# Kernel optimization log

Hardware: AMD Instinct MI355X
Metric: run time of the kernel (lower is better)

Reference implementation:

```python
import jax, jax.numpy as jnp
import numpy as np

IMG = 224          # image_size
FMAP = (56, 56)    # feature_map_dims (AdaptiveAvgPool2d((56,56)))
K_REWEIGHT = 3     # self.n_reweight
BLUR_RADIUS = 4    # KNNGaussianBlur(4): kernel 9, sigma 4


def _cdist(a, b):
    # Euclidean pairwise distance, [Na, D] x [Nb, D] -> [Na, Nb]
    a2 = jnp.sum(a * a, axis=1, keepdims=True)            # [Na,1]
    b2 = jnp.sum(b * b, axis=1, keepdims=True).T          # [1,Nb]
    d2 = a2 + b2 - 2.0 * (a @ b.T)
    return jnp.sqrt(jnp.maximum(d2, 0.0))


def _gaussian_blur(x):
    # x: [1,1,H,W]; torchvision GaussianBlur(kernel=9, sigma=4), reflect pad
    r, sigma = BLUR_RADIUS, float(BLUR_RADIUS)
    t = jnp.arange(2 * r + 1, dtype=x.dtype) - r
    g = jnp.exp(-(t * t) / (2.0 * sigma * sigma))
    g = g / jnp.sum(g)
    k2d = jnp.outer(g, g)[None, None]                     # [1,1,9,9]
    xp = jnp.pad(x, ((0, 0), (0, 0), (r, r), (r, r)), mode='reflect')
    return jax.lax.conv_general_dilated(
        xp, k2d, window_strides=(1, 1), padding='VALID',
        dimension_numbers=('NCHW', 'OIHW', 'NCHW'))


def setup_inputs() -> dict:
    key = jax.random.key(0)
    k1, k2 = jax.random.split(key)
    patch = jax.random.normal(k1, (FMAP[0] * FMAP[1], 768), dtype=jnp.float32)
    patch_lib = jax.random.normal(k2, (16384, 768), dtype=jnp.float32)
    mean = jnp.zeros((), dtype=jnp.float32)
    std = jnp.ones((), dtype=jnp.float32)
    return {"patch": patch, "patch_lib": patch_lib, "mean": mean, "std": std}


def reference(patch, patch_lib, mean, std):
    # normalization (method_name != 'Point_MAE' branch)
    p = (patch - mean) / std                               # [N, D]

    dist = _cdist(p, patch_lib)                            # [N, Nlib]
    min_val = jnp.min(dist, axis=1)                        # [N]
    min_idx = jnp.argmin(dist, axis=1)                     # [N]
    s_idx = jnp.argmax(min_val)
    s_star = jnp.max(min_val)

    m_test = p[s_idx]                                      # [D]
    m_star = patch_lib[min_idx[s_idx]]                     # [D]

    # distances of m_star to whole bank, k smallest
    w_dist = jnp.sqrt(jnp.maximum(
        jnp.sum((patch_lib - m_star) ** 2, axis=1), 0.0))  # [Nlib]
    _, nn_idx = jax.lax.top_k(-w_dist, K_REWEIGHT)         # smallest k
    m_star_knn = jnp.linalg.norm(
        m_test[None, :] - patch_lib[nn_idx[1:]], axis=1)   # [k-1]

    D_sqrt = jnp.sqrt(jnp.asarray(patch.shape[1], dtype=p.dtype))
    w = 1.0 - jnp.exp(s_star / D_sqrt) / jnp.sum(jnp.exp(m_star_knn / D_sqrt))
    s = w * s_star

    s_map = min_val.reshape(1, 1, *FMAP)
    s_map = jax.image.resize(s_map, (1, 1, IMG, IMG), method='bilinear')
    s_map = _gaussian_blur(s_map)
    return s, s_map
```

## Files before the change

### kernel.cpp

```cpp
#include <hip/hip_runtime.h>
#include <hip/hip_bf16.h>
#include <stdint.h>

#define N_PATCH 3136
#define N_PATCH_PAD 3328
#define N_LIB   16384
#define DIM     768
#define IMGSZ   224
#define FM      56

#define TILE 256
#define KT2 12
#define MT 13
#define NTILES 64

#define TAILB 64
#define D2_MARGIN 8.0f

typedef __bf16 bf16_t;
typedef __bf16 bf16x8 __attribute__((ext_vector_type(8)));
typedef __bf16 bf16x4_v __attribute__((ext_vector_type(4)));
typedef float  f32x4  __attribute__((ext_vector_type(4)));

#define FLT_MAX_ 3.402823466e+38f

struct Scal {
  unsigned long long approx_max_pack;
  unsigned long long cand_pack[64];
  int cand[64];
  int cand_count;
  int bar[4];
  int work;
};

__device__ __forceinline__ float wave_reduce_sum(float v) {
#pragma unroll
  for (int s = 32; s > 0; s >>= 1) v += __shfl_xor(v, s, 64);
  return v;
}

__device__ __forceinline__ float wave_reduce_min(float v) {
#pragma unroll
  for (int s = 32; s > 0; s >>= 1) v = fminf(v, __shfl_xor(v, s, 64));
  return v;
}

__device__ __forceinline__ unsigned long long shfl_xor_u64(unsigned long long v, int mask) {
  unsigned lo = (unsigned)v, hi = (unsigned)(v >> 32);
  lo = __shfl_xor(lo, mask, 64);
  hi = __shfl_xor(hi, mask, 64);
  return ((unsigned long long)hi << 32) | lo;
}

__device__ __forceinline__ void async16(const bf16_t* g, bf16_t* l) {
  __builtin_amdgcn_global_load_lds(
      (const __attribute__((address_space(1))) unsigned int*)g,
      (__attribute__((address_space(3))) unsigned int*)l, 16, 0, 0);
}

__device__ __forceinline__ void grid_bar(int* ctr, int nb) {
  __syncthreads();
  if (threadIdx.x == 0) {
    __threadfence();
    atomicAdd(ctr, 1);
    while (atomicAdd(ctr, 0) < nb) __builtin_amdgcn_s_sleep(8);
    __threadfence();
  }
  __syncthreads();
}

__device__ __forceinline__ float bf16u_to_f(unsigned short u) {
  return __uint_as_float(((unsigned)u) << 16);
}

__global__ void prep_kernel(const float* __restrict__ patch, const float* __restrict__ lib,
                            const float* __restrict__ meanp, const float* __restrict__ stdp,
                            bf16_t* __restrict__ pb, bf16_t* __restrict__ lb,
                            float* __restrict__ a2, float* __restrict__ b2, Scal* sc) {
  int t = threadIdx.x;
  int lane = t & 63;
  if (blockIdx.x == 0) {
    if (t < 64) sc->cand_pack[t] = ~0ULL;
    if (t == 64) { sc->approx_max_pack = 0ULL; sc->cand_count = 0; }
    if (t >= 65 && t < 69) sc->bar[t - 65] = 0;
    if (t == 69) sc->work = 0;
  }
  if (blockIdx.x < N_PATCH_PAD / 4) {
    int row = blockIdx.x * 4 + (t >> 6);
    if (row < N_PATCH) {
      float mu = meanp[0], sd = stdp[0];
      float acc = 0.f;
#pragma unroll
      for (int k = 0; k < 3; k++) {
        float4 v = ((const float4*)(patch + (size_t)row * DIM))[lane + 64 * k];
        v.x = (v.x - mu) / sd; v.y = (v.y - mu) / sd;
        v.z = (v.z - mu) / sd; v.w = (v.w - mu) / sd;
        bf16x4_v o = {(__bf16)v.x, (__bf16)v.y, (__bf16)v.z, (__bf16)v.w};
        *(bf16x4_v*)(pb + (size_t)row * DIM + (lane + 64 * k) * 4) = o;
        acc += v.x*v.x + v.y*v.y + v.z*v.z + v.w*v.w;
      }
      acc = wave_reduce_sum(acc);
      if (lane == 0) a2[row] = acc;
    } else {
      bf16x4_v z = {(__bf16)0.f, (__bf16)0.f, (__bf16)0.f, (__bf16)0.f};
#pragma unroll
      for (int k = 0; k < 3; k++)
        *(bf16x4_v*)(pb + (size_t)row * DIM + (lane + 64 * k) * 4) = z;
    }
  } else {
    int row = (blockIdx.x - N_PATCH_PAD / 4) * 4 + (t >> 6);
    float acc = 0.f;
#pragma unroll
    for (int k = 0; k < 3; k++) {
      float4 v = ((const float4*)(lib + (size_t)row * DIM))[lane + 64 * k];
      bf16x4_v o = {(__bf16)v.x, (__bf16)v.y, (__bf16)v.z, (__bf16)v.w};
      *(bf16x4_v*)(lb + (size_t)row * DIM + (lane + 64 * k) * 4) = o;
      acc += v.x*v.x + v.y*v.y + v.z*v.z + v.w*v.w;
    }
    acc = wave_reduce_sum(acc);
    if (lane == 0) b2[row] = acc;
  }
}

__global__ __launch_bounds__(512, 2)
void gemm_min_kernel(const bf16_t* __restrict__ pb, const bf16_t* __restrict__ lb,
                     const float* __restrict__ a2, const float* __restrict__ b2,
                     float* __restrict__ part) {
  __shared__ __align__(16) bf16_t As[2][2][128 * 64];
  __shared__ __align__(16) bf16_t Bs[2][2][128 * 64];

  const int t = threadIdx.x;
  const int wave = t >> 6;
  const int lane = t & 63;
  const int l15 = lane & 15;
  const int quad = lane >> 4;
  const int wm = (wave >> 2) * 128;
  const int wn = (wave & 3) * 64;
  const int mhw = wm >> 7;
  const int nhw = wn >> 7;
  const int wni = wn & 64;

  const int L0 = t >> 3;
  const int k0 = (t & 7) ^ (L0 & 7);
  const int sl0 = (((0 * 4 + quad) ^ (l15 & 7)) << 4);
  const int sl1 = (((1 * 4 + quad) ^ (l15 & 7)) << 4);

  const int x = blockIdx.x & 7;
  const int sblk = blockIdx.x >> 3;
  const int nt = x * 8 + (sblk & 7);
  const int n0 = nt * TILE;

  for (int g = 0; g < 4; ++g) {
    if (g * 32 + sblk >= 104) break;
    const int mt = g * 4 + (sblk >> 3);
    const int m0 = mt * TILE;

    __syncthreads();

    const bf16_t* gA = pb + (size_t)(m0 + L0) * DIM + k0 * 8;
    const bf16_t* gB = lb + (size_t)(n0 + L0) * DIM + k0 * 8;

    auto stageT = [&](int tk) {
      bf16_t* dA0 = &As[tk & 1][0][0];
      bf16_t* dA1 = &As[tk & 1][1][0];
      bf16_t* dB0 = &Bs[tk & 1][0][0];
      bf16_t* dB1 = &Bs[tk & 1][1][0];
      const bf16_t* sA = gA + tk * 64;
      const bf16_t* sB = gB + tk * 64;
      async16(sA,                       dA0 + t * 8);
      async16(sA + (size_t)64  * DIM,   dA0 + 4096 + t * 8);
      async16(sA + (size_t)128 * DIM,   dA1 + t * 8);
      async16(sA + (size_t)192 * DIM,   dA1 + 4096 + t * 8);
      async16(sB,                       dB0 + t * 8);
      async16(sB + (size_t)64  * DIM,   dB0 + 4096 + t * 8);
      async16(sB + (size_t)128 * DIM,   dB1 + t * 8);
      async16(sB + (size_t)192 * DIM,   dB1 + 4096 + t * 8);
    };

    f32x4 acc[8][4];
#pragma unroll
    for (int mi = 0; mi < 8; mi++)
#pragma unroll
      for (int ni = 0; ni < 4; ni++) { f32x4 z = {0.f,0.f,0.f,0.f}; acc[mi][ni] = z; }

    auto computeTile = [&](int d) {
      const char* Ab = (const char*)&As[d][mhw][0];
      const char* Bb = (const char*)&Bs[d][nhw][0];
      bf16x8 bfr[4][2];
#pragma unroll
      for (int ni = 0; ni < 4; ni++) {
        int lr = wni + ni * 16 + l15;
        bfr[ni][0] = *(const bf16x8*)(Bb + lr * 128 + sl0);
        bfr[ni][1] = *(const bf16x8*)(Bb + lr * 128 + sl1);
      }
#pragma unroll
      for (int q = 0; q < 4; q++) {
        bf16x8 aq[2][2];
#pragma unroll
        for (int mi = 0; mi < 2; mi++) {
          int lr = q * 32 + mi * 16 + l15;
          aq[mi][0] = *(const bf16x8*)(Ab + lr * 128 + sl0);
          aq[mi][1] = *(const bf16x8*)(Ab + lr * 128 + sl1);
        }
        __builtin_amdgcn_s_setprio(1);
#pragma unroll
        for (int mi = 0; mi < 2; mi++)
#pragma unroll
          for (int ni = 0; ni < 4; ni++) {
            acc[q*2+mi][ni] = __builtin_amdgcn_mfma_f32_16x16x32_bf16(
                aq[mi][0], bfr[ni][0], acc[q*2+mi][ni], 0, 0, 0);
            acc[q*2+mi][ni] = __builtin_amdgcn_mfma_f32_16x16x32_bf16(
                aq[mi][1], bfr[ni][1], acc[q*2+mi][ni], 0, 0, 0);
          }
        __builtin_amdgcn_s_setprio(0);
      }
    };

    stageT(0);
    for (int tk = 0; tk < KT2; ++tk) {
      asm volatile("s_waitcnt vmcnt(0) lgkmcnt(0)" ::: "memory");
      __builtin_amdgcn_s_barrier();
      asm volatile("" ::: "memory");
      if (tk + 1 < KT2) stageT(tk + 1);
      computeTile(tk & 1);
    }

    __syncthreads();
    unsigned* smin = (unsigned*)&As[0][0][0];
    if (t < 256) smin[t] = 0xffffffffu;
    __syncthreads();

    float b2n[4];
#pragma unroll
    for (int ni = 0; ni < 4; ni++) b2n[ni] = b2[n0 + wn + ni * 16 + l15];

#pragma unroll
    for (int mi = 0; mi < 8; mi++) {
#pragma unroll
      for (int r = 0; r < 4; r++) {
        int rloc = wm + mi * 16 + quad * 4 + r;
        int mrow = m0 + rloc;
        float a2v = a2[mrow < N_PATCH ? mrow : (N_PATCH - 1)];
        float best = a2v + b2n[0] - 2.0f * acc[mi][0][r];
#pragma unroll
        for (int ni = 1; ni < 4; ni++)
          best = fminf(best, a2v + b2n[ni] - 2.0f * acc[mi][ni][r]);
        best = fmaxf(best, 0.0f);
#pragma unroll
        for (int s = 1; s < 16; s <<= 1)
          best = fminf(best, __shfl_xor(best, s, 64));
        if (l15 == 0) atomicMin(&smin[rloc], __float_as_uint(best));
      }
    }
    __syncthreads();
    if (t < 256) part[(size_t)(m0 + t) * NTILES + nt] = __uint_as_float(smin[t]);
  }
}

__device__ __forceinline__ void wave_pick(const Scal* sc, int cnt, int lane,
                                          int* srow, float* sstar, int* ms) {
  unsigned long long pk = 0ULL;
  int rowv = 0, msv = 0;
  if (lane < cnt) {
    unsigned long long cp = sc->cand_pack[lane];
    rowv = sc->cand[lane];
    msv = (int)(cp & 0xffffffffu);
    pk = (cp & 0xffffffff00000000ULL) | (unsigned)(0xffffffffu - (unsigned)rowv);
  }
  unsigned long long m = pk;
#pragma unroll
  for (int s = 1; s < 64; s <<= 1) {
    unsigned long long o = shfl_xor_u64(m, s);
    if (o > m) m = o;
  }
  unsigned long long mask = __ballot(pk == m && lane < cnt);
  int wl = (int)(__ffsll((long long)mask) - 1);
  *srow = __shfl(rowv, wl, 64);
  *ms   = __shfl(msv, wl, 64);
  *sstar = sqrtf(__uint_as_float((unsigned)(m >> 32)));
}

__global__ __launch_bounds__(256, 2)
void tail_kernel(const float* __restrict__ part, float* __restrict__ min_val,
                 const float* __restrict__ patch, const float* __restrict__ lib,
                 const bf16_t* __restrict__ lb,
                 const float* __restrict__ meanp, const float* __restrict__ stdp,
                 Scal* __restrict__ sc, float* __restrict__ wdist2,
                 float* __restrict__ out0, float* __restrict__ outmap) {
  __shared__ union {
    unsigned long long sl[768];
    float rs[40 * 40];
  } sm;
  __shared__ float redbuf[4];
  __shared__ unsigned long long rb64[4];
  __shared__ int s_cnt;

  const int t = threadIdx.x;
  const int b = blockIdx.x;
  const int wave = t >> 6, lane = t & 63;

  {
    unsigned long long mp = 0ULL;
    for (int i = wave; i < 256; i += 4) {
      int row = b * 256 + i;
      if (row >= N_PATCH) break;
      float v = part[(size_t)row * NTILES + lane];
      v = wave_reduce_min(v);
      if (lane == 0) {
        float sv = sqrtf(v);
        min_val[row] = sv;
        unsigned long long cand = (((unsigned long long)__float_as_uint(sv)) << 32) |
                                  (unsigned)(0xffffffffu - (unsigned)row);
        if (cand > mp) mp = cand;
      }
    }
    if (lane == 0) rb64[wave] = mp;
    __syncthreads();
    if (t == 0) {
      unsigned long long mm = rb64[0];
      if (rb64[1] > mm) mm = rb64[1];
      if (rb64[2] > mm) mm = rb64[2];
      if (rb64[3] > mm) mm = rb64[3];
      if (mm) atomicMax(&sc->approx_max_pack, mm);
    }
  }
  grid_bar(&sc->bar[0], TAILB);

  if (b == 0) {
    float amax = __uint_as_float((unsigned)(atomicMax(&sc->approx_max_pack, 0ULL) >> 32));
    for (int i = t; i < N_PATCH; i += 256) {
      if (min_val[i] >= amax - 0.05f) {
        int p = atomicAdd(&sc->cand_count, 1);
        if (p < 64) sc->cand[p] = i;
      }
    }
  }
  grid_bar(&sc->bar[1], TAILB);

  if (t == 0) s_cnt = atomicAdd(&sc->cand_count, 0);
  __syncthreads();
  int cnt = s_cnt; if (cnt > 64) cnt = 64;

  {
    float mu = meanp[0], sd = stdp[0];
    for (int c = 0; c < cnt; c++) {
      int row = sc->cand[c];
      float pv_ = (t < NTILES) ? part[(size_t)row * NTILES + t] : FLT_MAX_;
      pv_ = wave_reduce_min(pv_);
      if (lane == 0) redbuf[wave] = pv_;
      __syncthreads();
      float bmin = fminf(fminf(redbuf[0], redbuf[1]), fminf(redbuf[2], redbuf[3]));
      __syncthreads();

      float4 pv[3];
#pragma unroll
      for (int k = 0; k < 3; k++) {
        float4 v = ((const float4*)(patch + (size_t)row * DIM))[lane + 64 * k];
        v.x = (v.x - mu) / sd; v.y = (v.y - mu) / sd;
        v.z = (v.z - mu) / sd; v.w = (v.w - mu) / sd;
        pv[k] = v;
      }
      int nt = b;
      float pmin = part[(size_t)row * NTILES + nt];
      if (pmin <= bmin + D2_MARGIN) {
        unsigned long long best = ~0ULL;
        int jb = nt * 256 + wave * 64;
        for (int rr = 0; rr < 64; rr++) {
          int j = jb + rr;
          const float4* pl = (const float4*)(lib + (size_t)j * DIM);
          float acc = 0.f;
#pragma unroll
          for (int k = 0; k < 3; k++) {
            float4 l = pl[lane + 64 * k];
            float dx = pv[k].x - l.x, dy = pv[k].y - l.y;
            float dz = pv[k].z - l.z, dw = pv[k].w - l.w;
            acc += dx*dx + dy*dy + dz*dz + dw*dw;
          }
          acc = wave_reduce_sum(acc);
          unsigned long long pk = (((unsigned long long)__float_as_uint(acc)) << 32) | (unsigned)j;
          if (pk < best) best = pk;
        }
        if (lane == 0) atomicMin(&sc->cand_pack[c], best);
      }
    }
  }
  grid_bar(&sc->bar[2], TAILB);

  {
    int srow_, ms; float ss_;
    wave_pick(sc, cnt, lane, &srow_, &ss_, &ms);
    float pm[12];
    const ushort4* pms = (const ushort4*)(lb + (size_t)ms * DIM);
#pragma unroll
    for (int k = 0; k < 3; k++) {
      ushort4 u = pms[lane + 64 * k];
      pm[k*4+0] = bf16u_to_f(u.x); pm[k*4+1] = bf16u_to_f(u.y);
      pm[k*4+2] = bf16u_to_f(u.z); pm[k*4+3] = bf16u_to_f(u.w);
    }
    int jbase = b * 256 + wave * 64;
    for (int rr = 0; rr < 64; rr += 2) {
      int j0 = jbase + rr, j1 = j0 + 1;
      const ushort4* r0 = (const ushort4*)(lb + (size_t)j0 * DIM);
      const ushort4* r1 = (const ushort4*)(lb + (size_t)j1 * DIM);
      float a0 = 0.f, a1 = 0.f;
#pragma unroll
      for (int k = 0; k < 3; k++) {
        ushort4 u0 = r0[lane + 64 * k];
        ushort4 u1 = r1[lane + 64 * k];
        float d;
        d = bf16u_to_f(u0.x) - pm[k*4+0]; a0 += d * d;
        d = bf16u_to_f(u0.y) - pm[k*4+1]; a0 += d * d;
        d = bf16u_to_f(u0.z) - pm[k*4+2]; a0 += d * d;
        d = bf16u_to_f(u0.w) - pm[k*4+3]; a0 += d * d;
        d = bf16u_to_f(u1.x) - pm[k*4+0]; a1 += d * d;
        d = bf16u_to_f(u1.y) - pm[k*4+1]; a1 += d * d;
        d = bf16u_to_f(u1.z) - pm[k*4+2]; a1 += d * d;
        d = bf16u_to_f(u1.w) - pm[k*4+3]; a1 += d * d;
      }
      a0 = wave_reduce_sum(a0);
      a1 = wave_reduce_sum(a1);
      if (lane == 0) { wdist2[j0] = a0; wdist2[j1] = a1; }
    }
  }
  grid_bar(&sc->bar[3], TAILB);

  if (b == 0) {
    unsigned long long b0 = ~0ULL, b1 = ~0ULL, b2 = ~0ULL;
    for (int j = t; j < N_LIB; j += 256) {
      unsigned long long pk = (((unsigned long long)__float_as_uint(wdist2[j])) << 32) | (unsigned)j;
      if (pk < b0)      { b2 = b1; b1 = b0; b0 = pk; }
      else if (pk < b1) { b2 = b1; b1 = pk; }
      else if (pk < b2) { b2 = pk; }
    }
    sm.sl[t * 3 + 0] = b0; sm.sl[t * 3 + 1] = b1; sm.sl[t * 3 + 2] = b2;
    __syncthreads();
    if (t >= 64) return;

    unsigned long long c0 = ~0ULL, c1 = ~0ULL, c2 = ~0ULL;
#pragma unroll
    for (int e = 0; e < 12; e++) {
      unsigned long long pk = sm.sl[t * 12 + e];
      if (pk < c0)      { c2 = c1; c1 = c0; c0 = pk; }
      else if (pk < c1) { c2 = c1; c1 = pk; }
      else if (pk < c2) { c2 = pk; }
    }
    unsigned long long res1 = 0, res2 = 0;
#pragma unroll
    for (int r = 0; r < 3; r++) {
      unsigned long long m = c0;
#pragma unroll
      for (int s = 1; s < 64; s <<= 1) {
        unsigned long long o = shfl_xor_u64(m, s);
        if (o < m) m = o;
      }
      if (r == 1) res1 = m;
      if (r == 2) res2 = m;
      if (c0 == m) { c0 = c1; c1 = c2; c2 = ~0ULL; }
    }
    int nA = (int)(res1 & 0xffffffffu);
    int nB = (int)(res2 & 0xffffffffu);

    int srow, ms2; float sstar;
    wave_pick(sc, cnt, t, &srow, &sstar, &ms2);

    float mu = meanp[0], sd = stdp[0];
    float accA = 0.f, accB = 0.f;
#pragma unroll
    for (int k = 0; k < 3; k++) {
      float4 p4 = ((const float4*)(patch + (size_t)srow * DIM))[t + 64 * k];
      float4 a4 = ((const float4*)(lib + (size_t)nA * DIM))[t + 64 * k];
      float4 b4 = ((const float4*)(lib + (size_t)nB * DIM))[t + 64 * k];
      float px = (p4.x - mu) / sd, py = (p4.y - mu) / sd;
      float pz = (p4.z - mu) / sd, pw = (p4.w - mu) / sd;
      float dax = px - a4.x, day = py - a4.y, daz = pz - a4.z, daw = pw - a4.w;
      float dbx = px - b4.x, dby = py - b4.y, dbz = pz - b4.z, dbw = pw - b4.w;
      accA += dax*dax + day*day + daz*daz + daw*daw;
      accB += dbx*dbx + dby*dby + dbz*dbz + dbw*dbw;
    }
    accA = wave_reduce_sum(accA);
    accB = wave_reduce_sum(accB);
    if (t == 0) {
      float dsq = sqrtf((float)DIM);
      float d1 = sqrtf(accA), d2v = sqrtf(accB);
      float w = 1.0f - expf(sstar / dsq) / (expf(d1 / dsq) + expf(d2v / dsq));
      out0[0] = w * sstar;
    }
    return;
  }

  if (b > 49) return;
  {
    int tile = b - 1;
    int bx = tile % 7, by = tile / 7;
    int ox0 = bx * 32, oy0 = by * 32;

    for (int i = t; i < 1600; i += 256) {
      int ly = i / 40, lx = i % 40;
      int gy = oy0 - 4 + ly; gy = gy < 0 ? 0 : (gy > 223 ? 223 : gy);
      int gx = ox0 - 4 + lx; gx = gx < 0 ? 0 : (gx > 223 ? 223 : gx);
      float sy = fminf(fmaxf(0.25f * gy - 0.375f, 0.0f), 55.0f);
      float sx = fminf(fmaxf(0.25f * gx - 0.375f, 0.0f), 55.0f);
      int y0 = (int)sy; if (y0 > 54) y0 = 54;
      int x0 = (int)sx; if (x0 > 54) x0 = 54;
      float fy = sy - y0, fx = sx - x0;
      float v00 = min_val[y0*FM + x0],     v01 = min_val[y0*FM + x0 + 1];
      float v10 = min_val[(y0+1)*FM + x0], v11 = min_val[(y0+1)*FM + x0 + 1];
      float a = v00 + fx * (v01 - v00);
      float bb = v10 + fx * (v11 - v10);
      sm.rs[i] = a + fy * (bb - a);
    }
    __syncthreads();

    float g[9]; float gs = 0.f;
#pragma unroll
    for (int i = 0; i < 9; i++) { float tt = (float)(i - 4); g[i] = expf(-(tt*tt)/32.0f); gs += g[i]; }
#pragma unroll
    for (int i = 0; i < 9; i++) g[i] /= gs;

    for (int p = t; p < 1024; p += 256) {
      int y = oy0 + p / 32, x = ox0 + (p & 31);
      float acc = 0.f;
#pragma unroll
      for (int dy = 0; dy < 9; dy++) {
        int yy = y + dy - 4;
        yy = yy < 0 ? -yy : (yy > IMGSZ - 1 ? 2*(IMGSZ-1) - yy : yy);
        int lyy = yy - (oy0 - 4);
        float ra = 0.f;
#pragma unroll
        for (int dx = 0; dx < 9; dx++) {
          int xx = x + dx - 4;
          xx = xx < 0 ? -xx : (xx > IMGSZ - 1 ? 2*(IMGSZ-1) - xx : xx);
          ra += g[dx] * sm.rs[lyy * 40 + (xx - (ox0 - 4))];
        }
        acc += g[dy] * ra;
      }
      outmap[y * IMGSZ + x] = acc;
    }
  }
}

extern "C" void kernel_launch(void* const* d_in, const int* in_sizes, int n_in,
                              void* d_out, int out_size, void* d_ws, size_t ws_size,
                              hipStream_t stream) {
  const float* patch = (const float*)d_in[0];
  const float* lib   = (const float*)d_in[1];
  const float* meanp = (const float*)d_in[2];
  const float* stdp  = (const float*)d_in[3];
  float* out = (float*)d_out;

  char* ws = (char*)d_ws;
  size_t off = 0;
  auto alloc = [&](size_t bytes) -> void* {
    void* p = ws + off;
    off = (off + bytes + 255) & ~(size_t)255;
    return p;
  };
  bf16_t* pb      = (bf16_t*)alloc((size_t)N_PATCH_PAD * DIM * sizeof(bf16_t));
  bf16_t* lb      = (bf16_t*)alloc((size_t)N_LIB * DIM * sizeof(bf16_t));
  float* a2       = (float*)alloc(N_PATCH * sizeof(float));
  float* b2       = (float*)alloc(N_LIB * sizeof(float));
  float* part     = (float*)alloc((size_t)N_PATCH_PAD * NTILES * sizeof(float));
  float* min_val  = (float*)alloc(N_PATCH * sizeof(float));
  float* wdist2   = (float*)alloc(N_LIB * sizeof(float));
  Scal*  sc       = (Scal*)alloc(sizeof(Scal));

  prep_kernel<<<N_PATCH_PAD / 4 + N_LIB / 4, 256, 0, stream>>>(patch, lib, meanp, stdp,
                                                               pb, lb, a2, b2, sc);
  gemm_min_kernel<<<256, 512, 0, stream>>>(pb, lb, a2, b2, part);
  tail_kernel<<<TAILB, 256, 0, stream>>>(part, min_val, patch, lib, lb, meanp, stdp,
                                         sc, wdist2, out, out + 1);
}
```

Baseline: 349.7 us.

## Fuse prep, GEMM-min and tail into one cooperative persistent kernel

Merges the three kernels (bf16 conversion/norms, GEMM with row-min, and the tail reductions, reweighting and blur) into one cooperative kernel with 256 blocks of 512 threads. Phases are separated by grid barriers, and the tail work is spread over all 256 blocks instead of 64. The goal is to remove two kernel launch gaps and use more of the GPU for the latency-bound tail phases. In exchange it adds six grid-wide barriers plus a memset, and the prep phase now runs under the GEMM's launch bounds and LDS footprint.

```diff
diff --git a/kernel.cpp b/kernel.cpp
--- a/kernel.cpp
+++ b/kernel.cpp
@@ -14,7 +14,7 @@
 #define MT 13
 #define NTILES 64
 
-#define TAILB 64
+#define GRID 256
 #define D2_MARGIN 8.0f
 
 typedef __bf16 bf16_t;
@@ -29,8 +29,7 @@
   unsigned long long cand_pack[64];
   int cand[64];
   int cand_count;
-  int bar[4];
-  int work;
+  int bar[6];
 };
 
 __device__ __forceinline__ float wave_reduce_sum(float v) {
@@ -71,190 +70,6 @@
 
 __device__ __forceinline__ float bf16u_to_f(unsigned short u) {
   return __uint_as_float(((unsigned)u) << 16);
-}
-
-__global__ void prep_kernel(const float* __restrict__ patch, const float* __restrict__ lib,
-                            const float* __restrict__ meanp, const float* __restrict__ stdp,
-                            bf16_t* __restrict__ pb, bf16_t* __restrict__ lb,
-                            float* __restrict__ a2, float* __restrict__ b2, Scal* sc) {
-  int t = threadIdx.x;
-  int lane = t & 63;
-  if (blockIdx.x == 0) {
-    if (t < 64) sc->cand_pack[t] = ~0ULL;
-    if (t == 64) { sc->approx_max_pack = 0ULL; sc->cand_count = 0; }
-    if (t >= 65 && t < 69) sc->bar[t - 65] = 0;
-    if (t == 69) sc->work = 0;
-  }
-  if (blockIdx.x < N_PATCH_PAD / 4) {
-    int row = blockIdx.x * 4 + (t >> 6);
-    if (row < N_PATCH) {
-      float mu = meanp[0], sd = stdp[0];
-      float acc = 0.f;
-#pragma unroll
-      for (int k = 0; k < 3; k++) {
-        float4 v = ((const float4*)(patch + (size_t)row * DIM))[lane + 64 * k];
-        v.x = (v.x - mu) / sd; v.y = (v.y - mu) / sd;
-        v.z = (v.z - mu) / sd; v.w = (v.w - mu) / sd;
-        bf16x4_v o = {(__bf16)v.x, (__bf16)v.y, (__bf16)v.z, (__bf16)v.w};
-        *(bf16x4_v*)(pb + (size_t)row * DIM + (lane + 64 * k) * 4) = o;
-        acc += v.x*v.x + v.y*v.y + v.z*v.z + v.w*v.w;
-      }
-      acc = wave_reduce_sum(acc);
-      if (lane == 0) a2[row] = acc;
-    } else {
-      bf16x4_v z = {(__bf16)0.f, (__bf16)0.f, (__bf16)0.f, (__bf16)0.f};
-#pragma unroll
-      for (int k = 0; k < 3; k++)
-        *(bf16x4_v*)(pb + (size_t)row * DIM + (lane + 64 * k) * 4) = z;
-    }
-  } else {
-    int row = (blockIdx.x - N_PATCH_PAD / 4) * 4 + (t >> 6);
-    float acc = 0.f;
-#pragma unroll
-    for (int k = 0; k < 3; k++) {
-      float4 v = ((const float4*)(lib + (size_t)row * DIM))[lane + 64 * k];
-      bf16x4_v o = {(__bf16)v.x, (__bf16)v.y, (__bf16)v.z, (__bf16)v.w};
-      *(bf16x4_v*)(lb + (size_t)row * DIM + (lane + 64 * k) * 4) = o;
-      acc += v.x*v.x + v.y*v.y + v.z*v.z + v.w*v.w;
-    }
-    acc = wave_reduce_sum(acc);
-    if (lane == 0) b2[row] = acc;
-  }
-}
-
-__global__ __launch_bounds__(512, 2)
-void gemm_min_kernel(const bf16_t* __restrict__ pb, const bf16_t* __restrict__ lb,
-                     const float* __restrict__ a2, const float* __restrict__ b2,
-                     float* __restrict__ part) {
-  __shared__ __align__(16) bf16_t As[2][2][128 * 64];
-  __shared__ __align__(16) bf16_t Bs[2][2][128 * 64];
-
-  const int t = threadIdx.x;
-  const int wave = t >> 6;
-  const int lane = t & 63;
-  const int l15 = lane & 15;
-  const int quad = lane >> 4;
-  const int wm = (wave >> 2) * 128;
-  const int wn = (wave & 3) * 64;
-  const int mhw = wm >> 7;
-  const int nhw = wn >> 7;
-  const int wni = wn & 64;
-
-  const int L0 = t >> 3;
-  const int k0 = (t & 7) ^ (L0 & 7);
-  const int sl0 = (((0 * 4 + quad) ^ (l15 & 7)) << 4);
-  const int sl1 = (((1 * 4 + quad) ^ (l15 & 7)) << 4);
-
-  const int x = blockIdx.x & 7;
-  const int sblk = blockIdx.x >> 3;
-  const int nt = x * 8 + (sblk & 7);
-  const int n0 = nt * TILE;
-
-  for (int g = 0; g < 4; ++g) {
-    if (g * 32 + sblk >= 104) break;
-    const int mt = g * 4 + (sblk >> 3);
-    const int m0 = mt * TILE;
-
-    __syncthreads();
-
-    const bf16_t* gA = pb + (size_t)(m0 + L0) * DIM + k0 * 8;
-    const bf16_t* gB = lb + (size_t)(n0 + L0) * DIM + k0 * 8;
-
-    auto stageT = [&](int tk) {
-      bf16_t* dA0 = &As[tk & 1][0][0];
-      bf16_t* dA1 = &As[tk & 1][1][0];
-      bf16_t* dB0 = &Bs[tk & 1][0][0];
-      bf16_t* dB1 = &Bs[tk & 1][1][0];
-      const bf16_t* sA = gA + tk * 64;
-      const bf16_t* sB = gB + tk * 64;
-      async16(sA,                       dA0 + t * 8);
-      async16(sA + (size_t)64  * DIM,   dA0 + 4096 + t * 8);
-      async16(sA + (size_t)128 * DIM,   dA1 + t * 8);
-      async16(sA + (size_t)192 * DIM,   dA1 + 4096 + t * 8);
-      async16(sB,                       dB0 + t * 8);
-      async16(sB + (size_t)64  * DIM,   dB0 + 4096 + t * 8);
-      async16(sB + (size_t)128 * DIM,   dB1 + t * 8);
-      async16(sB + (size_t)192 * DIM,   dB1 + 4096 + t * 8);
-    };
-
-    f32x4 acc[8][4];
-#pragma unroll
-    for (int mi = 0; mi < 8; mi++)
-#pragma unroll
-      for (int ni = 0; ni < 4; ni++) { f32x4 z = {0.f,0.f,0.f,0.f}; acc[mi][ni] = z; }
-
-    auto computeTile = [&](int d) {
-      const char* Ab = (const char*)&As[d][mhw][0];
-      const char* Bb = (const char*)&Bs[d][nhw][0];
-      bf16x8 bfr[4][2];
-#pragma unroll
-      for (int ni = 0; ni < 4; ni++) {
-        int lr = wni + ni * 16 + l15;
-        bfr[ni][0] = *(const bf16x8*)(Bb + lr * 128 + sl0);
-        bfr[ni][1] = *(const bf16x8*)(Bb + lr * 128 + sl1);
-      }
-#pragma unroll
-      for (int q = 0; q < 4; q++) {
-        bf16x8 aq[2][2];
-#pragma unroll
-        for (int mi = 0; mi < 2; mi++) {
-          int lr = q * 32 + mi * 16 + l15;
-          aq[mi][0] = *(const bf16x8*)(Ab + lr * 128 + sl0);
-          aq[mi][1] = *(const bf16x8*)(Ab + lr * 128 + sl1);
-        }
-        __builtin_amdgcn_s_setprio(1);
-#pragma unroll
-        for (int mi = 0; mi < 2; mi++)
-#pragma unroll
-          for (int ni = 0; ni < 4; ni++) {
-            acc[q*2+mi][ni] = __builtin_amdgcn_mfma_f32_16x16x32_bf16(
-                aq[mi][0], bfr[ni][0], acc[q*2+mi][ni], 0, 0, 0);
-            acc[q*2+mi][ni] = __builtin_amdgcn_mfma_f32_16x16x32_bf16(
-                aq[mi][1], bfr[ni][1], acc[q*2+mi][ni], 0, 0, 0);
-          }
-        __builtin_amdgcn_s_setprio(0);
-      }
-    };
-
-    stageT(0);
-    for (int tk = 0; tk < KT2; ++tk) {
-      asm volatile("s_waitcnt vmcnt(0) lgkmcnt(0)" ::: "memory");
-      __builtin_amdgcn_s_barrier();
-      asm volatile("" ::: "memory");
-      if (tk + 1 < KT2) stageT(tk + 1);
-      computeTile(tk & 1);
-    }
-
-    __syncthreads();
-    unsigned* smin = (unsigned*)&As[0][0][0];
-    if (t < 256) smin[t] = 0xffffffffu;
-    __syncthreads();
-
-    float b2n[4];
-#pragma unroll
-    for (int ni = 0; ni < 4; ni++) b2n[ni] = b2[n0 + wn + ni * 16 + l15];
-
-#pragma unroll
-    for (int mi = 0; mi < 8; mi++) {
-#pragma unroll
-      for (int r = 0; r < 4; r++) {
-        int rloc = wm + mi * 16 + quad * 4 + r;
-        int mrow = m0 + rloc;
-        float a2v = a2[mrow < N_PATCH ? mrow : (N_PATCH - 1)];
-        float best = a2v + b2n[0] - 2.0f * acc[mi][0][r];
-#pragma unroll
-        for (int ni = 1; ni < 4; ni++)
-          best = fminf(best, a2v + b2n[ni] - 2.0f * acc[mi][ni][r]);
-        best = fmaxf(best, 0.0f);
-#pragma unroll
-        for (int s = 1; s < 16; s <<= 1)
-          best = fminf(best, __shfl_xor(best, s, 64));
-        if (l15 == 0) atomicMin(&smin[rloc], __float_as_uint(best));
-      }
-    }
-    __syncthreads();
-    if (t < 256) part[(size_t)(m0 + t) * NTILES + nt] = __uint_as_float(smin[t]);
-  }
 }
 
 __device__ __forceinline__ void wave_pick(const Scal* sc, int cnt, int lane,
@@ -280,30 +95,196 @@
   *sstar = sqrtf(__uint_as_float((unsigned)(m >> 32)));
 }
 
-__global__ __launch_bounds__(256, 2)
-void tail_kernel(const float* __restrict__ part, float* __restrict__ min_val,
-                 const float* __restrict__ patch, const float* __restrict__ lib,
-                 const bf16_t* __restrict__ lb,
+__global__ __launch_bounds__(512, 2)
+void mega_kernel(const float* __restrict__ patch, const float* __restrict__ lib,
                  const float* __restrict__ meanp, const float* __restrict__ stdp,
-                 Scal* __restrict__ sc, float* __restrict__ wdist2,
+                 bf16_t* __restrict__ pb, bf16_t* __restrict__ lb,
+                 float* __restrict__ a2, float* __restrict__ b2,
+                 float* __restrict__ part, float* __restrict__ min_val,
+                 float* __restrict__ wdist2, Scal* __restrict__ sc,
                  float* __restrict__ out0, float* __restrict__ outmap) {
-  __shared__ union {
-    unsigned long long sl[768];
-    float rs[40 * 40];
-  } sm;
-  __shared__ float redbuf[4];
-  __shared__ unsigned long long rb64[4];
+  __shared__ __align__(16) bf16_t As[2][2][128 * 64];
+  __shared__ __align__(16) bf16_t Bs[2][2][128 * 64];
+  __shared__ unsigned long long rb64[8];
   __shared__ int s_cnt;
 
   const int t = threadIdx.x;
+  const int wave = t >> 6;
+  const int lane = t & 63;
+  const int l15 = lane & 15;
+  const int quad = lane >> 4;
   const int b = blockIdx.x;
-  const int wave = t >> 6, lane = t & 63;
+  const int gw = b * 8 + wave;
+
+  if (b == 0 && t < 64) sc->cand_pack[t] = ~0ULL;
+  {
+    float mu = meanp[0], sd = stdp[0];
+    for (int r = gw; r < N_PATCH_PAD + N_LIB; r += 2048) {
+      if (r < N_PATCH_PAD) {
+        if (r < N_PATCH) {
+          float acc = 0.f;
+#pragma unroll
+          for (int k = 0; k < 3; k++) {
+            float4 v = ((const float4*)(patch + (size_t)r * DIM))[lane + 64 * k];
+            v.x = (v.x - mu) / sd; v.y = (v.y - mu) / sd;
+            v.z = (v.z - mu) / sd; v.w = (v.w - mu) / sd;
+            bf16x4_v o = {(__bf16)v.x, (__bf16)v.y, (__bf16)v.z, (__bf16)v.w};
+            *(bf16x4_v*)(pb + (size_t)r * DIM + (lane + 64 * k) * 4) = o;
+            acc += v.x*v.x + v.y*v.y + v.z*v.z + v.w*v.w;
+          }
+          acc = wave_reduce_sum(acc);
+          if (lane == 0) a2[r] = acc;
+        } else {
+          bf16x4_v z = {(__bf16)0.f, (__bf16)0.f, (__bf16)0.f, (__bf16)0.f};
+#pragma unroll
+          for (int k = 0; k < 3; k++)
+            *(bf16x4_v*)(pb + (size_t)r * DIM + (lane + 64 * k) * 4) = z;
+        }
+      } else {
+        int row = r - N_PATCH_PAD;
+        float acc = 0.f;
+#pragma unroll
+        for (int k = 0; k < 3; k++) {
+          float4 v = ((const float4*)(lib + (size_t)row * DIM))[lane + 64 * k];
+          bf16x4_v o = {(__bf16)v.x, (__bf16)v.y, (__bf16)v.z, (__bf16)v.w};
+          *(bf16x4_v*)(lb + (size_t)row * DIM + (lane + 64 * k) * 4) = o;
+          acc += v.x*v.x + v.y*v.y + v.z*v.z + v.w*v.w;
+        }
+        acc = wave_reduce_sum(acc);
+        if (lane == 0) b2[row] = acc;
+      }
+    }
+  }
+  grid_bar(&sc->bar[0], GRID);
+
+  {
+    const int wm = (wave >> 2) * 128;
+    const int wn = (wave & 3) * 64;
+    const int mhw = wm >> 7;
+    const int nhw = wn >> 7;
+    const int wni = wn & 64;
+
+    const int L0 = t >> 3;
+    const int k0 = (t & 7) ^ (L0 & 7);
+    const int sl0 = (((0 * 4 + quad) ^ (l15 & 7)) << 4);
+    const int sl1 = (((1 * 4 + quad) ^ (l15 & 7)) << 4);
+
+    const int x = b & 7;
+    const int sblk = b >> 3;
+    const int nt = x * 8 + (sblk & 7);
+    const int n0 = nt * TILE;
+
+    for (int g = 0; g < 4; ++g) {
+      if (g * 32 + sblk >= 104) break;
+      const int mt = g * 4 + (sblk >> 3);
+      const int m0 = mt * TILE;
+
+      __syncthreads();
+
+      const bf16_t* gA = pb + (size_t)(m0 + L0) * DIM + k0 * 8;
+      const bf16_t* gB = lb + (size_t)(n0 + L0) * DIM + k0 * 8;
+
+      auto stageT = [&](int tk) {
+        bf16_t* dA0 = &As[tk & 1][0][0];
+        bf16_t* dA1 = &As[tk & 1][1][0];
+        bf16_t* dB0 = &Bs[tk & 1][0][0];
+        bf16_t* dB1 = &Bs[tk & 1][1][0];
+        const bf16_t* sA = gA + tk * 64;
+        const bf16_t* sB = gB + tk * 64;
+        async16(sA,                       dA0 + t * 8);
+        async16(sA + (size_t)64  * DIM,   dA0 + 4096 + t * 8);
+        async16(sA + (size_t)128 * DIM,   dA1 + t * 8);
+        async16(sA + (size_t)192 * DIM,   dA1 + 4096 + t * 8);
+        async16(sB,                       dB0 + t * 8);
+        async16(sB + (size_t)64  * DIM,   dB0 + 4096 + t * 8);
+        async16(sB + (size_t)128 * DIM,   dB1 + t * 8);
+        async16(sB + (size_t)192 * DIM,   dB1 + 4096 + t * 8);
+      };
+
+      f32x4 acc[8][4];
+#pragma unroll
+      for (int mi = 0; mi < 8; mi++)
+#pragma unroll
+        for (int ni = 0; ni < 4; ni++) { f32x4 z = {0.f,0.f,0.f,0.f}; acc[mi][ni] = z; }
+
+      auto computeTile = [&](int d) {
+        const char* Ab = (const char*)&As[d][mhw][0];
+        const char* Bb = (const char*)&Bs[d][nhw][0];
+        bf16x8 bfr[4][2];
+#pragma unroll
+        for (int ni = 0; ni < 4; ni++) {
+          int lr = wni + ni * 16 + l15;
+          bfr[ni][0] = *(const bf16x8*)(Bb + lr * 128 + sl0);
+          bfr[ni][1] = *(const bf16x8*)(Bb + lr * 128 + sl1);
+        }
+#pragma unroll
+        for (int q = 0; q < 4; q++) {
+          bf16x8 aq[2][2];
+#pragma unroll
+          for (int mi = 0; mi < 2; mi++) {
+            int lr = q * 32 + mi * 16 + l15;
+            aq[mi][0] = *(const bf16x8*)(Ab + lr * 128 + sl0);
+            aq[mi][1] = *(const bf16x8*)(Ab + lr * 128 + sl1);
+          }
+          __builtin_amdgcn_s_setprio(1);
+#pragma unroll
+          for (int mi = 0; mi < 2; mi++)
+#pragma unroll
+            for (int ni = 0; ni < 4; ni++) {
+              acc[q*2+mi][ni] = __builtin_amdgcn_mfma_f32_16x16x32_bf16(
+                  aq[mi][0], bfr[ni][0], acc[q*2+mi][ni], 0, 0, 0);
+              acc[q*2+mi][ni] = __builtin_amdgcn_mfma_f32_16x16x32_bf16(
+                  aq[mi][1], bfr[ni][1], acc[q*2+mi][ni], 0, 0, 0);
+            }
+          __builtin_amdgcn_s_setprio(0);
+        }
+      };
+
+      stageT(0);
+      for (int tk = 0; tk < KT2; ++tk) {
+        asm volatile("s_waitcnt vmcnt(0) lgkmcnt(0)" ::: "memory");
+        __builtin_amdgcn_s_barrier();
+        asm volatile("" ::: "memory");
+        if (tk + 1 < KT2) stageT(tk + 1);
+        computeTile(tk & 1);
+      }
+
+      __syncthreads();
+      unsigned* smin = (unsigned*)&As[0][0][0];
+      if (t < 256) smin[t] = 0xffffffffu;
+      __syncthreads();
+
+      float b2n[4];
+#pragma unroll
+      for (int ni = 0; ni < 4; ni++) b2n[ni] = b2[n0 + wn + ni * 16 + l15];
+
+#pragma unroll
+      for (int mi = 0; mi < 8; mi++) {
+#pragma unroll
+        for (int r = 0; r < 4; r++) {
+          int rloc = wm + mi * 16 + quad * 4 + r;
+          int mrow = m0 + rloc;
+          float a2v = a2[mrow < N_PATCH ? mrow : (N_PATCH - 1)];
+          float best = a2v + b2n[0] - 2.0f * acc[mi][0][r];
+#pragma unroll
+          for (int ni = 1; ni < 4; ni++)
+            best = fminf(best, a2v + b2n[ni] - 2.0f * acc[mi][ni][r]);
+          best = fmaxf(best, 0.0f);
+#pragma unroll
+          for (int s = 1; s < 16; s <<= 1)
+            best = fminf(best, __shfl_xor(best, s, 64));
+          if (l15 == 0) atomicMin(&smin[rloc], __float_as_uint(best));
+        }
+      }
+      __syncthreads();
+      if (t < 256) part[(size_t)(m0 + t) * NTILES + nt] = __uint_as_float(smin[t]);
+    }
+  }
+  grid_bar(&sc->bar[1], GRID);
 
   {
     unsigned long long mp = 0ULL;
-    for (int i = wave; i < 256; i += 4) {
-      int row = b * 256 + i;
-      if (row >= N_PATCH) break;
+    for (int row = gw; row < N_PATCH; row += 2048) {
       float v = part[(size_t)row * NTILES + lane];
       v = wave_reduce_min(v);
       if (lane == 0) {
@@ -318,24 +299,23 @@
     __syncthreads();
     if (t == 0) {
       unsigned long long mm = rb64[0];
-      if (rb64[1] > mm) mm = rb64[1];
-      if (rb64[2] > mm) mm = rb64[2];
-      if (rb64[3] > mm) mm = rb64[3];
+#pragma unroll
+      for (int w = 1; w < 8; w++) if (rb64[w] > mm) mm = rb64[w];
       if (mm) atomicMax(&sc->approx_max_pack, mm);
     }
   }
-  grid_bar(&sc->bar[0], TAILB);
+  grid_bar(&sc->bar[2], GRID);
 
   if (b == 0) {
     float amax = __uint_as_float((unsigned)(atomicMax(&sc->approx_max_pack, 0ULL) >> 32));
-    for (int i = t; i < N_PATCH; i += 256) {
+    for (int i = t; i < N_PATCH; i += 512) {
       if (min_val[i] >= amax - 0.05f) {
         int p = atomicAdd(&sc->cand_count, 1);
         if (p < 64) sc->cand[p] = i;
       }
     }
   }
-  grid_bar(&sc->bar[1], TAILB);
+  grid_bar(&sc->bar[3], GRID);
 
   if (t == 0) s_cnt = atomicAdd(&sc->cand_count, 0);
   __syncthreads();
@@ -343,29 +323,25 @@
 
   {
     float mu = meanp[0], sd = stdp[0];
+    const int nt2 = b >> 2;
+    const int qt = b & 3;
     for (int c = 0; c < cnt; c++) {
       int row = sc->cand[c];
-      float pv_ = (t < NTILES) ? part[(size_t)row * NTILES + t] : FLT_MAX_;
-      pv_ = wave_reduce_min(pv_);
-      if (lane == 0) redbuf[wave] = pv_;
-      __syncthreads();
-      float bmin = fminf(fminf(redbuf[0], redbuf[1]), fminf(redbuf[2], redbuf[3]));
-      __syncthreads();
-
-      float4 pv[3];
-#pragma unroll
-      for (int k = 0; k < 3; k++) {
-        float4 v = ((const float4*)(patch + (size_t)row * DIM))[lane + 64 * k];
-        v.x = (v.x - mu) / sd; v.y = (v.y - mu) / sd;
-        v.z = (v.z - mu) / sd; v.w = (v.w - mu) / sd;
-        pv[k] = v;
-      }
-      int nt = b;
-      float pmin = part[(size_t)row * NTILES + nt];
+      float pv_ = part[(size_t)row * NTILES + lane];
+      float bmin = wave_reduce_min(pv_);
+      float pmin = part[(size_t)row * NTILES + nt2];
       if (pmin <= bmin + D2_MARGIN) {
+        float4 pv[3];
+#pragma unroll
+        for (int k = 0; k < 3; k++) {
+          float4 v = ((const float4*)(patch + (size_t)row * DIM))[lane + 64 * k];
+          v.x = (v.x - mu) / sd; v.y = (v.y - mu) / sd;
+          v.z = (v.z - mu) / sd; v.w = (v.w - mu) / sd;
+          pv[k] = v;
+        }
         unsigned long long best = ~0ULL;
-        int jb = nt * 256 + wave * 64;
-        for (int rr = 0; rr < 64; rr++) {
+        int jb = nt2 * 256 + qt * 64 + wave * 8;
+        for (int rr = 0; rr < 8; rr++) {
           int j = jb + rr;
           const float4* pl = (const float4*)(lib + (size_t)j * DIM);
           float acc = 0.f;
@@ -384,7 +360,7 @@
       }
     }
   }
-  grid_bar(&sc->bar[2], TAILB);
+  grid_bar(&sc->bar[4], GRID);
 
   {
     int srow_, ms; float ss_;
@@ -397,8 +373,8 @@
       pm[k*4+0] = bf16u_to_f(u.x); pm[k*4+1] = bf16u_to_f(u.y);
       pm[k*4+2] = bf16u_to_f(u.z); pm[k*4+3] = bf16u_to_f(u.w);
     }
-    int jbase = b * 256 + wave * 64;
-    for (int rr = 0; rr < 64; rr += 2) {
+    int jbase = gw * 8;
+    for (int rr = 0; rr < 8; rr += 2) {
       int j0 = jbase + rr, j1 = j0 + 1;
       const ushort4* r0 = (const ushort4*)(lb + (size_t)j0 * DIM);
       const ushort4* r1 = (const ushort4*)(lb + (size_t)j1 * DIM);
@@ -422,24 +398,25 @@
       if (lane == 0) { wdist2[j0] = a0; wdist2[j1] = a1; }
     }
   }
-  grid_bar(&sc->bar[3], TAILB);
+  grid_bar(&sc->bar[5], GRID);
 
   if (b == 0) {
+    unsigned long long* sl = (unsigned long long*)&Bs[0][0][0];
     unsigned long long b0 = ~0ULL, b1 = ~0ULL, b2 = ~0ULL;
-    for (int j = t; j < N_LIB; j += 256) {
+    for (int j = t; j < N_LIB; j += 512) {
       unsigned long long pk = (((unsigned long long)__float_as_uint(wdist2[j])) << 32) | (unsigned)j;
       if (pk < b0)      { b2 = b1; b1 = b0; b0 = pk; }
       else if (pk < b1) { b2 = b1; b1 = pk; }
       else if (pk < b2) { b2 = pk; }
     }
-    sm.sl[t * 3 + 0] = b0; sm.sl[t * 3 + 1] = b1; sm.sl[t * 3 + 2] = b2;
+    sl[t * 3 + 0] = b0; sl[t * 3 + 1] = b1; sl[t * 3 + 2] = b2;
     __syncthreads();
     if (t >= 64) return;
 
     unsigned long long c0 = ~0ULL, c1 = ~0ULL, c2 = ~0ULL;
 #pragma unroll
-    for (int e = 0; e < 12; e++) {
-      unsigned long long pk = sm.sl[t * 12 + e];
+    for (int e = 0; e < 24; e++) {
+      unsigned long long pk = sl[t * 24 + e];
       if (pk < c0)      { c2 = c1; c1 = c0; c0 = pk; }
       else if (pk < c1) { c2 = c1; c1 = pk; }
       else if (pk < c2) { c2 = pk; }
@@ -490,11 +467,12 @@
 
   if (b > 49) return;
   {
+    float* rs = (float*)&Bs[0][0][0];
     int tile = b - 1;
     int bx = tile % 7, by = tile / 7;
     int ox0 = bx * 32, oy0 = by * 32;
 
-    for (int i = t; i < 1600; i += 256) {
+    for (int i = t; i < 1600; i += 512) {
       int ly = i / 40, lx = i % 40;
       int gy = oy0 - 4 + ly; gy = gy < 0 ? 0 : (gy > 223 ? 223 : gy);
       int gx = ox0 - 4 + lx; gx = gx < 0 ? 0 : (gx > 223 ? 223 : gx);
@@ -507,7 +485,7 @@
       float v10 = min_val[(y0+1)*FM + x0], v11 = min_val[(y0+1)*FM + x0 + 1];
       float a = v00 + fx * (v01 - v00);
       float bb = v10 + fx * (v11 - v10);
-      sm.rs[i] = a + fy * (bb - a);
+      rs[i] = a + fy * (bb - a);
     }
     __syncthreads();
 
@@ -517,7 +495,7 @@
 #pragma unroll
     for (int i = 0; i < 9; i++) g[i] /= gs;
 
-    for (int p = t; p < 1024; p += 256) {
+    for (int p = t; p < 1024; p += 512) {
       int y = oy0 + p / 32, x = ox0 + (p & 31);
       float acc = 0.f;
 #pragma unroll
@@ -530,7 +508,7 @@
         for (int dx = 0; dx < 9; dx++) {
           int xx = x + dx - 4;
           xx = xx < 0 ? -xx : (xx > IMGSZ - 1 ? 2*(IMGSZ-1) - xx : xx);
-          ra += g[dx] * sm.rs[lyy * 40 + (xx - (ox0 - 4))];
+          ra += g[dx] * rs[lyy * 40 + (xx - (ox0 - 4))];
         }
         acc += g[dy] * ra;
       }
@@ -564,9 +542,15 @@
   float* wdist2   = (float*)alloc(N_LIB * sizeof(float));
   Scal*  sc       = (Scal*)alloc(sizeof(Scal));
 
-  prep_kernel<<<N_PATCH_PAD / 4 + N_LIB / 4, 256, 0, stream>>>(patch, lib, meanp, stdp,
-                                                               pb, lb, a2, b2, sc);
-  gemm_min_kernel<<<256, 512, 0, stream>>>(pb, lb, a2, b2, part);
-  tail_kernel<<<TAILB, 256, 0, stream>>>(part, min_val, patch, lib, lb, meanp, stdp,
-                                         sc, wdist2, out, out + 1);
-}
+  float* out0   = out;
+  float* outmap = out + 1;
+
+  hipMemsetAsync(sc, 0, sizeof(Scal), stream);
+
+  void* args[] = {(void*)&patch, (void*)&lib, (void*)&meanp, (void*)&stdp,
+                  (void*)&pb, (void*)&lb, (void*)&a2, (void*)&b2,
+                  (void*)&part, (void*)&min_val, (void*)&wdist2, (void*)&sc,
+                  (void*)&out0, (void*)&outmap};
+  hipLaunchCooperativeKernel((const void*)mega_kernel, dim3(GRID), dim3(512),
+                             args, 0, stream);
+}
```

After: 381.8 us. 1.09x slower.
